# Performance work log

Hardware: AMD Instinct MI355X
Metric: run time of the kernel (lower is better)

The kernel has to match this reference:

```python
import jax, jax.numpy as jnp
import numpy as np

B, L, H, HEADS, E, MPD = 4, 1024, 768, 12, 22, 128  # batch, seq, hidden, heads, entities/doc, mentions/doc
EMB = 512
M = B * MPD
NE = B * E


def setup_inputs() -> dict:
    key = jax.random.key(0)
    k1, k2, k3, k4, k5 = jax.random.split(key, 5)
    sequence_output = jax.random.normal(k1, (B, L, H), jnp.float32)
    # attention rows are softmax-normalized like real transformer attention
    attention = jax.nn.softmax(jax.random.normal(k2, (B, HEADS, L, L), jnp.float32), axis=-1)
    mention_batch = jnp.repeat(jnp.arange(B, dtype=jnp.int32), MPD)
    mention_pos = jax.random.randint(k3, (M,), 0, L, jnp.int32)
    local = jax.random.randint(k4, (M,), 0, E, jnp.int32)
    # guarantee every entity has >=1 mention (first E mentions of each doc cover 0..E-1)
    within = jnp.arange(M, dtype=jnp.int32) % MPD
    local = jnp.where(within < E, within, local)
    mention_entity = mention_batch * E + local
    w_trans = jax.random.normal(k5, (H, EMB), jnp.float32) * 0.02
    b_trans = jnp.zeros((EMB,), jnp.float32)
    return {
        "sequence_output": sequence_output,
        "attention": attention,
        "w_trans": w_trans,
        "b_trans": b_trans,
        "mention_batch": mention_batch,
        "mention_pos": mention_pos,
        "mention_entity": mention_entity,
    }


def reference(sequence_output, attention, w_trans, b_trans,
              mention_batch, mention_pos, mention_entity):
    # --- gather mention reps / attention rows (make_graph inner loop, vectorized) ---
    m_emb = sequence_output[mention_batch, mention_pos]          # [M, H]
    m_att = attention[mention_batch, :, mention_pos, :]          # [M, HEADS, L]

    counts = jax.ops.segment_sum(jnp.ones((M,), jnp.float32), mention_entity,
                                 num_segments=NE)                # [NE]
    has = counts > 0

    # entity embedding = logsumexp over that entity's mentions (stable segment version)
    mx = jax.ops.segment_max(m_emb, mention_entity, num_segments=NE)
    mx = jnp.where(has[:, None], mx, 0.0)
    sums = jax.ops.segment_sum(jnp.exp(m_emb - mx[mention_entity]), mention_entity,
                               num_segments=NE)
    entity_emb = jnp.where(has[:, None], jnp.log(sums + 1e-30) + mx, 0.0)  # [NE, H]

    # entity attention = mean over mentions, then mean over heads, then L1-normalize
    e_att = jax.ops.segment_sum(m_att, mention_entity, num_segments=NE)
    e_att = e_att / (counts[:, None, None] + 1e-5)               # [NE, HEADS, L]
    e_att = e_att.mean(axis=1)                                   # [NE, L]
    e_att = e_att / (e_att.sum(axis=1, keepdims=True) + 1e-5)

    # context pooling: e_context = e_att @ sequence_output (relation_map einsum)
    e_att_b = e_att.reshape(B, E, L)
    e_context = jnp.einsum("bel,blh->beh", e_att_b, sequence_output)  # [B, E, H]

    e_cg = e_context + entity_emb.reshape(B, E, H)
    out = jnp.tanh(e_cg @ w_trans + b_trans)                     # [B, E, EMB]
    return out
```

## Files before the change

### kernel.cpp

```cpp
#include <hip/hip_runtime.h>
#include <hip/hip_bf16.h>
#include <float.h>

#define B 4
#define L 1024
#define H 768
#define HEADS 12
#define E 22
#define MPD 128
#define EMB 512
#define M (B*MPD)
#define NE (B*E)

__global__ __launch_bounds__(256) void k_entity_emb(
    const float* __restrict__ seq, const int* __restrict__ m_batch,
    const int* __restrict__ m_pos, const int* __restrict__ m_ent,
    float* __restrict__ e_cg)
{
    const int e = blockIdx.x;
    const int t = threadIdx.x;
    __shared__ int s_idx[MPD];
    __shared__ int s_cnt;
    if (t == 0) s_cnt = 0;
    __syncthreads();
    for (int m = t; m < M; m += 256)
        if (m_ent[m] == e) { int p = atomicAdd(&s_cnt, 1); s_idx[p] = m; }
    __syncthreads();
    const int cnt = s_cnt;
    __shared__ size_t s_off[MPD];
    for (int i = t; i < cnt; i += 256) {
        int m = s_idx[i];
        s_off[i] = ((size_t)m_batch[m] * L + m_pos[m]) * H;
    }
    __syncthreads();

    float mx0 = -FLT_MAX, mx1 = -FLT_MAX, mx2 = -FLT_MAX;
    for (int i = 0; i < cnt; ++i) {
        const float* r = seq + s_off[i];
        mx0 = fmaxf(mx0, r[t]);
        mx1 = fmaxf(mx1, r[t + 256]);
        mx2 = fmaxf(mx2, r[t + 512]);
    }
    float s0 = 0.f, s1 = 0.f, s2 = 0.f;
    for (int i = 0; i < cnt; ++i) {
        const float* r = seq + s_off[i];
        s0 += expf(r[t]       - mx0);
        s1 += expf(r[t + 256] - mx1);
        s2 += expf(r[t + 512] - mx2);
    }
    float o0, o1, o2;
    if (cnt > 0) {
        o0 = logf(s0 + 1e-30f) + mx0;
        o1 = logf(s1 + 1e-30f) + mx1;
        o2 = logf(s2 + 1e-30f) + mx2;
    } else { o0 = o1 = o2 = 0.f; }
    float* dst = e_cg + (size_t)e * H;
    dst[t] = o0; dst[t + 256] = o1; dst[t + 512] = o2;
}

__global__ __launch_bounds__(1024) void k_eatt(
    const float* __restrict__ att, const int* __restrict__ m_batch,
    const int* __restrict__ m_pos, const int* __restrict__ m_ent,
    float* __restrict__ e_att)
{
    const int e = blockIdx.x;
    const int t = threadIdx.x;
    __shared__ int s_idx[MPD];
    __shared__ int s_cnt;
    if (t == 0) s_cnt = 0;
    __syncthreads();
    for (int m = t; m < M; m += 1024)
        if (m_ent[m] == e) { int p = atomicAdd(&s_cnt, 1); s_idx[p] = m; }
    __syncthreads();
    const int cnt = s_cnt;
    __shared__ size_t s_base[MPD];
    for (int i = t; i < cnt; i += 1024) {
        int m = s_idx[i];
        s_base[i] = (size_t)m_batch[m] * HEADS * L * L + (size_t)m_pos[m] * L;
    }
    __syncthreads();

    float acc = 0.f;
    for (int i = 0; i < cnt; ++i) {
        const size_t base = s_base[i] + t;
        #pragma unroll
        for (int hd = 0; hd < HEADS; ++hd)
            acc += att[base + (size_t)hd * ((size_t)L * L)];
    }
    const float denom = ((float)cnt + 1e-5f) * (float)HEADS;
    const float a1 = acc / denom;

    float v = a1;
    #pragma unroll
    for (int off = 32; off > 0; off >>= 1) v += __shfl_xor(v, off, 64);
    __shared__ float s_part[16];
    const int wid = t >> 6, lane = t & 63;
    if (lane == 0) s_part[wid] = v;
    __syncthreads();
    __shared__ float s_total;
    if (t == 0) {
        float tot = 0.f;
        #pragma unroll
        for (int w = 0; w < 16; ++w) tot += s_part[w];
        s_total = tot + 1e-5f;
    }
    __syncthreads();
    e_att[(size_t)e * L + t] = a1 / s_total;
}

__global__ __launch_bounds__(128) void k_econtext(
    const float* __restrict__ seq, const float* __restrict__ e_att,
    float* __restrict__ e_cg)
{
    const int b  = blockIdx.z;
    const int h  = blockIdx.x * 128 + threadIdx.x;
    const int l0 = blockIdx.y * 128;
    __shared__ float s_att[E][128];
    for (int i = threadIdx.x; i < E * 128; i += 128) {
        int el = i >> 7, dl = i & 127;
        s_att[el][dl] = e_att[(size_t)(b * E + el) * L + l0 + dl];
    }
    __syncthreads();
    float acc[E];
    #pragma unroll
    for (int e = 0; e < E; ++e) acc[e] = 0.f;
    const float* sp = seq + ((size_t)b * L + l0) * H + h;
    #pragma unroll 4
    for (int dl = 0; dl < 128; ++dl) {
        float s = sp[(size_t)dl * H];
        #pragma unroll
        for (int e = 0; e < E; ++e) acc[e] += s_att[e][dl] * s;
    }
    float* dst = e_cg + (size_t)(b * E) * H + h;
    #pragma unroll
    for (int e = 0; e < E; ++e) atomicAdd(dst + (size_t)e * H, acc[e]);
}

__global__ __launch_bounds__(512) void k_out(
    const float* __restrict__ e_cg, const float* __restrict__ w,
    const float* __restrict__ bias, float* __restrict__ out)
{
    const int row = blockIdx.x;
    const int c = threadIdx.x;
    __shared__ float s_row[H];
    for (int i = c; i < H; i += 512) s_row[i] = e_cg[(size_t)row * H + i];
    __syncthreads();
    float acc = bias[c];
    #pragma unroll 4
    for (int h = 0; h < H; ++h)
        acc += s_row[h] * w[(size_t)h * EMB + c];
    out[(size_t)row * EMB + c] = tanhf(acc);
}

extern "C" void kernel_launch(void* const* d_in, const int* in_sizes, int n_in,
                              void* d_out, int out_size, void* d_ws, size_t ws_size,
                              hipStream_t stream) {
    const float* seq   = (const float*)d_in[0];
    const float* att   = (const float*)d_in[1];
    const float* w     = (const float*)d_in[2];
    const float* bias  = (const float*)d_in[3];
    const int* m_batch = (const int*)d_in[4];
    const int* m_pos   = (const int*)d_in[5];
    const int* m_ent   = (const int*)d_in[6];
    float* out = (float*)d_out;

    float* ws    = (float*)d_ws;
    float* e_att = ws;
    float* e_cg  = ws + (size_t)NE * L;

    k_entity_emb<<<NE, 256, 0, stream>>>(seq, m_batch, m_pos, m_ent, e_cg);
    k_eatt<<<NE, 1024, 0, stream>>>(att, m_batch, m_pos, m_ent, e_att);
    dim3 g3(H / 128, L / 128, B);
    k_econtext<<<g3, 128, 0, stream>>>(seq, e_att, e_cg);
    k_out<<<NE, 512, 0, stream>>>(e_cg, w, bias, out);
}
```

Baseline: 374.8 us.

## Merge gather kernels, split attention by L-chunks, fold normalization into context

Merges the entity-embedding and entity-attention gather kernels into one launch. The attention part is split into four L-chunks per entity so more blocks are in flight, and each chunk writes a partial sum. The attention normalization (count and L1 sum) is deferred into the context kernel as a per-entity scale applied to the atomics. The context kernel also uses finer L chunks (16) and the output GEMV is split across column blocks, all to raise occupancy. The trade-off is one fewer launch and more parallelism against extra workspace, redundant mention scans per chunk, and more atomics into e_cg.

Result: faster. 320.0 us (-14.6%).

```diff
diff --git a/kernel.cpp b/kernel.cpp
--- a/kernel.cpp
+++ b/kernel.cpp
@@ -11,114 +11,109 @@
 #define EMB 512
 #define M (B*MPD)
 #define NE (B*E)
+#define LCH_A 4
+#define LCH_B 16
+#define LB (L/LCH_B)
 
-__global__ __launch_bounds__(256) void k_entity_emb(
-    const float* __restrict__ seq, const int* __restrict__ m_batch,
-    const int* __restrict__ m_pos, const int* __restrict__ m_ent,
+__global__ __launch_bounds__(256) void k_gather(
+    const float* __restrict__ seq, const float* __restrict__ att,
+    const int* __restrict__ m_batch, const int* __restrict__ m_pos,
+    const int* __restrict__ m_ent,
+    float* __restrict__ e_att_raw, float* __restrict__ e_cg,
+    float* __restrict__ zpart, float* __restrict__ cntf)
+{
+    const int bx = blockIdx.x;
+    const int t  = threadIdx.x;
+    __shared__ int s_cnt;
+    __shared__ size_t s_off[MPD];
+    __shared__ float s_p[4];
+    if (t == 0) s_cnt = 0;
+    __syncthreads();
+
+    if (bx < NE * LCH_A) {
+        const int e = bx >> 2, chunk = bx & 3;
+        for (int m = t; m < M; m += 256)
+            if (m_ent[m] == e) {
+                int p = atomicAdd(&s_cnt, 1);
+                s_off[p] = (size_t)m_batch[m] * HEADS * L * L + (size_t)m_pos[m] * L;
+            }
+        __syncthreads();
+        const int cnt = s_cnt;
+        const int l = chunk * 256 + t;
+        float acc = 0.f;
+        for (int i = 0; i < cnt; ++i) {
+            const float* p = att + s_off[i] + l;
+            #pragma unroll
+            for (int hd = 0; hd < HEADS; ++hd)
+                acc += p[(size_t)hd * L * L];
+        }
+        e_att_raw[(size_t)e * L + l] = acc;
+        float v = acc;
+        #pragma unroll
+        for (int off = 32; off > 0; off >>= 1) v += __shfl_xor(v, off, 64);
+        if ((t & 63) == 0) s_p[t >> 6] = v;
+        __syncthreads();
+        if (t == 0) {
+            zpart[bx] = s_p[0] + s_p[1] + s_p[2] + s_p[3];
+            if (chunk == 0) cntf[e] = (float)cnt;
+        }
+    } else {
+        const int e = bx - NE * LCH_A;
+        for (int m = t; m < M; m += 256)
+            if (m_ent[m] == e) {
+                int p = atomicAdd(&s_cnt, 1);
+                s_off[p] = ((size_t)m_batch[m] * L + m_pos[m]) * H;
+            }
+        __syncthreads();
+        const int cnt = s_cnt;
+        float mx0 = -FLT_MAX, mx1 = -FLT_MAX, mx2 = -FLT_MAX;
+        for (int i = 0; i < cnt; ++i) {
+            const float* r = seq + s_off[i];
+            mx0 = fmaxf(mx0, r[t]);
+            mx1 = fmaxf(mx1, r[t + 256]);
+            mx2 = fmaxf(mx2, r[t + 512]);
+        }
+        float s0 = 0.f, s1 = 0.f, s2 = 0.f;
+        for (int i = 0; i < cnt; ++i) {
+            const float* r = seq + s_off[i];
+            s0 += expf(r[t]       - mx0);
+            s1 += expf(r[t + 256] - mx1);
+            s2 += expf(r[t + 512] - mx2);
+        }
+        float o0, o1, o2;
+        if (cnt > 0) {
+            o0 = logf(s0 + 1e-30f) + mx0;
+            o1 = logf(s1 + 1e-30f) + mx1;
+            o2 = logf(s2 + 1e-30f) + mx2;
+        } else { o0 = o1 = o2 = 0.f; }
+        float* dst = e_cg + (size_t)e * H;
+        dst[t] = o0; dst[t + 256] = o1; dst[t + 512] = o2;
+    }
+}
+
+__global__ __launch_bounds__(128) void k_context(
+    const float* __restrict__ seq, const float* __restrict__ e_att_raw,
+    const float* __restrict__ zpart, const float* __restrict__ cntf,
     float* __restrict__ e_cg)
 {
-    const int e = blockIdx.x;
-    const int t = threadIdx.x;
-    __shared__ int s_idx[MPD];
-    __shared__ int s_cnt;
-    if (t == 0) s_cnt = 0;
-    __syncthreads();
-    for (int m = t; m < M; m += 256)
-        if (m_ent[m] == e) { int p = atomicAdd(&s_cnt, 1); s_idx[p] = m; }
-    __syncthreads();
-    const int cnt = s_cnt;
-    __shared__ size_t s_off[MPD];
-    for (int i = t; i < cnt; i += 256) {
-        int m = s_idx[i];
-        s_off[i] = ((size_t)m_batch[m] * L + m_pos[m]) * H;
+    const int ht = blockIdx.x;
+    const int lc = blockIdx.y;
+    const int b  = blockIdx.z;
+    const int t  = threadIdx.x;
+    const int h  = ht * 128 + t;
+    const int l0 = lc * LB;
+    __shared__ float s_att[E][LB];
+    __shared__ float s_norm[E];
+    for (int i = t; i < E * LB; i += 128) {
+        int el = i / LB, dl = i % LB;
+        s_att[el][dl] = e_att_raw[(size_t)(b * E + el) * L + l0 + dl];
     }
-    __syncthreads();
-
-    float mx0 = -FLT_MAX, mx1 = -FLT_MAX, mx2 = -FLT_MAX;
-    for (int i = 0; i < cnt; ++i) {
-        const float* r = seq + s_off[i];
-        mx0 = fmaxf(mx0, r[t]);
-        mx1 = fmaxf(mx1, r[t + 256]);
-        mx2 = fmaxf(mx2, r[t + 512]);
-    }
-    float s0 = 0.f, s1 = 0.f, s2 = 0.f;
-    for (int i = 0; i < cnt; ++i) {
-        const float* r = seq + s_off[i];
-        s0 += expf(r[t]       - mx0);
-        s1 += expf(r[t + 256] - mx1);
-        s2 += expf(r[t + 512] - mx2);
-    }
-    float o0, o1, o2;
-    if (cnt > 0) {
-        o0 = logf(s0 + 1e-30f) + mx0;
-        o1 = logf(s1 + 1e-30f) + mx1;
-        o2 = logf(s2 + 1e-30f) + mx2;
-    } else { o0 = o1 = o2 = 0.f; }
-    float* dst = e_cg + (size_t)e * H;
-    dst[t] = o0; dst[t + 256] = o1; dst[t + 512] = o2;
-}
-
-__global__ __launch_bounds__(1024) void k_eatt(
-    const float* __restrict__ att, const int* __restrict__ m_batch,
-    const int* __restrict__ m_pos, const int* __restrict__ m_ent,
-    float* __restrict__ e_att)
-{
-    const int e = blockIdx.x;
-    const int t = threadIdx.x;
-    __shared__ int s_idx[MPD];
-    __shared__ int s_cnt;
-    if (t == 0) s_cnt = 0;
-    __syncthreads();
-    for (int m = t; m < M; m += 1024)
-        if (m_ent[m] == e) { int p = atomicAdd(&s_cnt, 1); s_idx[p] = m; }
-    __syncthreads();
-    const int cnt = s_cnt;
-    __shared__ size_t s_base[MPD];
-    for (int i = t; i < cnt; i += 1024) {
-        int m = s_idx[i];
-        s_base[i] = (size_t)m_batch[m] * HEADS * L * L + (size_t)m_pos[m] * L;
-    }
-    __syncthreads();
-
-    float acc = 0.f;
-    for (int i = 0; i < cnt; ++i) {
-        const size_t base = s_base[i] + t;
-        #pragma unroll
-        for (int hd = 0; hd < HEADS; ++hd)
-            acc += att[base + (size_t)hd * ((size_t)L * L)];
-    }
-    const float denom = ((float)cnt + 1e-5f) * (float)HEADS;
-    const float a1 = acc / denom;
-
-    float v = a1;
-    #pragma unroll
-    for (int off = 32; off > 0; off >>= 1) v += __shfl_xor(v, off, 64);
-    __shared__ float s_part[16];
-    const int wid = t >> 6, lane = t & 63;
-    if (lane == 0) s_part[wid] = v;
-    __syncthreads();
-    __shared__ float s_total;
-    if (t == 0) {
-        float tot = 0.f;
-        #pragma unroll
-        for (int w = 0; w < 16; ++w) tot += s_part[w];
-        s_total = tot + 1e-5f;
-    }
-    __syncthreads();
-    e_att[(size_t)e * L + t] = a1 / s_total;
-}
-
-__global__ __launch_bounds__(128) void k_econtext(
-    const float* __restrict__ seq, const float* __restrict__ e_att,
-    float* __restrict__ e_cg)
-{
-    const int b  = blockIdx.z;
-    const int h  = blockIdx.x * 128 + threadIdx.x;
-    const int l0 = blockIdx.y * 128;
-    __shared__ float s_att[E][128];
-    for (int i = threadIdx.x; i < E * 128; i += 128) {
-        int el = i >> 7, dl = i & 127;
-        s_att[el][dl] = e_att[(size_t)(b * E + el) * L + l0 + dl];
+    if (t < E) {
+        int ge = b * E + t;
+        float z = zpart[ge * LCH_A] + zpart[ge * LCH_A + 1]
+                + zpart[ge * LCH_A + 2] + zpart[ge * LCH_A + 3];
+        float c2 = (cntf[ge] + 1e-5f) * (float)HEADS;
+        s_norm[t] = 1.f / (z + 1e-5f * c2);
     }
     __syncthreads();
     float acc[E];
@@ -126,27 +121,27 @@
     for (int e = 0; e < E; ++e) acc[e] = 0.f;
     const float* sp = seq + ((size_t)b * L + l0) * H + h;
     #pragma unroll 4
-    for (int dl = 0; dl < 128; ++dl) {
+    for (int dl = 0; dl < LB; ++dl) {
         float s = sp[(size_t)dl * H];
         #pragma unroll
         for (int e = 0; e < E; ++e) acc[e] += s_att[e][dl] * s;
     }
     float* dst = e_cg + (size_t)(b * E) * H + h;
     #pragma unroll
-    for (int e = 0; e < E; ++e) atomicAdd(dst + (size_t)e * H, acc[e]);
+    for (int e = 0; e < E; ++e) atomicAdd(dst + (size_t)e * H, acc[e] * s_norm[e]);
 }
 
-__global__ __launch_bounds__(512) void k_out(
+__global__ __launch_bounds__(128) void k_out(
     const float* __restrict__ e_cg, const float* __restrict__ w,
     const float* __restrict__ bias, float* __restrict__ out)
 {
     const int row = blockIdx.x;
-    const int c = threadIdx.x;
+    const int c   = blockIdx.y * 128 + threadIdx.x;
     __shared__ float s_row[H];
-    for (int i = c; i < H; i += 512) s_row[i] = e_cg[(size_t)row * H + i];
+    for (int i = threadIdx.x; i < H; i += 128) s_row[i] = e_cg[(size_t)row * H + i];
     __syncthreads();
     float acc = bias[c];
-    #pragma unroll 4
+    #pragma unroll 8
     for (int h = 0; h < H; ++h)
         acc += s_row[h] * w[(size_t)h * EMB + c];
     out[(size_t)row * EMB + c] = tanhf(acc);
@@ -164,13 +159,16 @@
     const int* m_ent   = (const int*)d_in[6];
     float* out = (float*)d_out;
 
-    float* ws    = (float*)d_ws;
-    float* e_att = ws;
-    float* e_cg  = ws + (size_t)NE * L;
+    float* ws        = (float*)d_ws;
+    float* e_att_raw = ws;
+    float* e_cg      = ws + (size_t)NE * L;
+    float* zpart     = e_cg + (size_t)NE * H;
+    float* cntf      = zpart + NE * LCH_A;
 
-    k_entity_emb<<<NE, 256, 0, stream>>>(seq, m_batch, m_pos, m_ent, e_cg);
-    k_eatt<<<NE, 1024, 0, stream>>>(att, m_batch, m_pos, m_ent, e_att);
-    dim3 g3(H / 128, L / 128, B);
-    k_econtext<<<g3, 128, 0, stream>>>(seq, e_att, e_cg);
-    k_out<<<NE, 512, 0, stream>>>(e_cg, w, bias, out);
+    k_gather<<<NE * LCH_A + NE, 256, 0, stream>>>(
+        seq, att, m_batch, m_pos, m_ent, e_att_raw, e_cg, zpart, cntf);
+    dim3 gB(H / 128, LCH_B, B);
+    k_context<<<gB, 128, 0, stream>>>(seq, e_att_raw, zpart, cntf, e_cg);
+    dim3 gC(NE, EMB / 128);
+    k_out<<<gC, 128, 0, stream>>>(e_cg, w, bias, out);
 }
```
